# Kernel tuning notes

Hardware: AMD Instinct MI355X
Metric: run time of the kernel (lower is better)

Reference implementation:

```python
import jax, jax.numpy as jnp
import numpy as np

B, N, M, D = 1, 16384, 16384, 3
CHUNK = 2048          # x tile size for the online-min KNN pass
NN_WEIGHT = 1.0       # self.nn_weight
# both_ways=False, free_weight=0, ch_normals_K=0 -> only cham_x branch is active


def setup_inputs() -> dict:
    key = jax.random.key(0)
    k1, k2, k3 = jax.random.split(key, 3)
    # LiDAR-like point clouds, scaled to a ~20 m scene extent
    pc1 = jax.random.normal(k1, (B, N, D), dtype=jnp.float32) * 10.0
    est_flow = jax.random.normal(k2, (B, N, D), dtype=jnp.float32) * 0.1
    pc2 = jax.random.normal(k3, (B, M, D), dtype=jnp.float32) * 10.0
    return {"pc1": pc1, "est_flow": est_flow, "pc2": pc2}


def _knn1_l1_dists(x, y):
    """Per-point min L1 distance from x [N,3] to y [M,3], tiled over x.

    Equivalent to knn_points(x, y, K=1, norm=1).dists[..., 0] without
    materializing the full [N, M] distance matrix.
    """
    n = x.shape[0]
    x_tiles = x.reshape(n // CHUNK, CHUNK, D)

    def tile_min(xc):  # xc: [CHUNK, 3]
        d = jnp.sum(jnp.abs(xc[:, None, :] - y[None, :, :]), axis=-1)  # [CHUNK, M]
        return jnp.min(d, axis=-1)                                     # [CHUNK]

    return jax.lax.map(tile_min, x_tiles).reshape(n)


def reference(pc1, est_flow, pc2):
    x = pc1 + est_flow                                   # deformed cloud [B,N,3]
    cham_x = jax.vmap(_knn1_l1_dists)(x, pc2)            # [B, N]
    cham_y = jnp.float32(0.0)                            # both_ways=False
    freespace_loss = jnp.zeros_like(cham_x)              # free_weight == 0 branch
    chamf_loss = NN_WEIGHT * (cham_x.mean() + cham_y)    # free_weight * 0 omitted
    return (chamf_loss, freespace_loss)
```

## Files before the change

### kernel.cpp

```cpp
#include <hip/hip_runtime.h>


#define TPB 256
#define RB 8
#define PTS_PER_BLOCK (TPB * RB)
#define YSEG 128

__device__ __forceinline__ float rl(float v, int l) {
    return __uint_as_float((unsigned)__builtin_amdgcn_readlane((int)__float_as_uint(v), l));
}

#define DIST2S(MR, AXv, AYv, AZv, Y0X, Y0Y, Y0Z, Y1X, Y1Y, Y1Z)           \
  {                                                                        \
    float t0, t1, t2, t3, t4;                                              \
    asm("v_sub_f32 %1, %9, %6\n\t"                                         \
        "v_sub_f32 %2, %10, %7\n\t"                                        \
        "v_sub_f32 %3, %11, %8\n\t"                                        \
        "v_sub_f32 %4, %12, %6\n\t"                                        \
        "v_sub_f32 %5, %13, %7\n\t"                                        \
        "v_add_f32 %1, |%1|, |%2|\n\t"                                     \
        "v_sub_f32 %2, %14, %8\n\t"                                        \
        "v_add_f32 %4, |%4|, |%5|\n\t"                                     \
        "v_add_f32 %1, %1, |%3|\n\t"                                       \
        "v_add_f32 %4, %4, |%2|\n\t"                                       \
        "v_min3_f32 %0, %0, %1, %4"                                        \
        : "+v"(MR), "=&v"(t0), "=&v"(t1), "=&v"(t2), "=&v"(t3), "=&v"(t4)  \
        : "v"(AXv), "v"(AYv), "v"(AZv),                                    \
          "s"(Y0X), "s"(Y0Y), "s"(Y0Z), "s"(Y1X), "s"(Y1Y), "s"(Y1Z));    \
  }

__global__ __launch_bounds__(TPB) void init_kernel(unsigned* __restrict__ minbits, int N) {
    const int i = blockIdx.x * TPB + threadIdx.x;
    uint4* p = (uint4*)minbits;
    if (i < N / 4) p[i] = make_uint4(0x7F7F7F7Fu, 0x7F7F7F7Fu, 0x7F7F7F7Fu, 0x7F7F7F7Fu);
    for (int k = (N / 4) * 4 + i; k < N; k += 1) { if (i == 0) minbits[k] = 0x7F7F7F7Fu; }
}

__global__ __launch_bounds__(TPB) void chamfer_kernel(
    const float* __restrict__ pc1, const float* __restrict__ flow,
    const float* __restrict__ pc2, unsigned* __restrict__ minbits,
    int N, int M) {
    const int t    = threadIdx.x;
    const int lane = t & 63;

    const int ibase = blockIdx.x * PTS_PER_BLOCK + t;
    float ax[RB], ay[RB], az[RB];
#pragma unroll
    for (int r = 0; r < RB; ++r) {
        const int i = ibase + r * TPB;
        const int ic = (i < N) ? i : (N - 1);
        ax[r] = pc1[3 * ic]     + flow[3 * ic];
        ay[r] = pc1[3 * ic + 1] + flow[3 * ic + 1];
        az[r] = pc1[3 * ic + 2] + flow[3 * ic + 2];
    }

    float m[RB];
#pragma unroll
    for (int r = 0; r < RB; ++r) m[r] = 3.0e38f;

    const int ybase = blockIdx.y * YSEG;
    const int yend  = (ybase + YSEG < M) ? (ybase + YSEG) : M;
    const int nph   = (yend - ybase + 63) >> 6;

    int g = ybase + lane; if (g >= M) g = M - 1;
    float cyx = pc2[3 * g], cyy = pc2[3 * g + 1], cyz = pc2[3 * g + 2];

    for (int p = 0; p < nph; ++p) {
        float nyx, nyy, nyz;
        const bool more = (p + 1 < nph);
        if (more) {
            int h = ybase + (p + 1) * 64 + lane; if (h >= M) h = M - 1;
            nyx = pc2[3 * h]; nyy = pc2[3 * h + 1]; nyz = pc2[3 * h + 2];
        }
#pragma unroll
        for (int j = 0; j < 64; j += 2) {
            const float y0x = rl(cyx, j),     y0y = rl(cyy, j),     y0z = rl(cyz, j);
            const float y1x = rl(cyx, j + 1), y1y = rl(cyy, j + 1), y1z = rl(cyz, j + 1);
#pragma unroll
            for (int r = 0; r < RB; ++r) {
                DIST2S(m[r], ax[r], ay[r], az[r], y0x, y0y, y0z, y1x, y1y, y1z);
            }
        }
        if (more) { cyx = nyx; cyy = nyy; cyz = nyz; }
    }

#pragma unroll
    for (int r = 0; r < RB; ++r) {
        const int i = ibase + r * TPB;
        if (i < N) atomicMin(&minbits[i], __float_as_uint(m[r]));
    }
}

__global__ __launch_bounds__(1024) void reduce_kernel(
    const unsigned* __restrict__ minbits, float* __restrict__ out,
    int N, int out_size) {
    float4* o4 = (float4*)out;
    const int n4 = out_size / 4;
    for (int k = threadIdx.x; k < n4; k += 1024)
        o4[k] = make_float4(0.f, 0.f, 0.f, 0.f);
    for (int k = n4 * 4 + threadIdx.x; k < out_size; k += 1024)
        out[k] = 0.f;

    float s = 0.0f;
    const uint4* p = (const uint4*)minbits;
    for (int k = threadIdx.x; k < N / 4; k += 1024) {
        uint4 v = p[k];
        s += __uint_as_float(v.x) + __uint_as_float(v.y) +
             __uint_as_float(v.z) + __uint_as_float(v.w);
    }
    for (int k = (N / 4) * 4 + threadIdx.x; k < N; k += 1024)
        s += __uint_as_float(minbits[k]);
#pragma unroll
    for (int off = 32; off > 0; off >>= 1) s += __shfl_down(s, off, 64);
    __shared__ float ls[16];
    const int wid = threadIdx.x >> 6, lane = threadIdx.x & 63;
    if (lane == 0) ls[wid] = s;
    __syncthreads();
    if (threadIdx.x == 0) {
        float tot = 0.0f;
        for (int w = 0; w < 16; ++w) tot += ls[w];
        out[0] = tot / (float)N;
    }
}

extern "C" void kernel_launch(void* const* d_in, const int* in_sizes, int n_in,
                              void* d_out, int out_size, void* d_ws, size_t ws_size,
                              hipStream_t stream) {
    const float* pc1  = (const float*)d_in[0];
    const float* flow = (const float*)d_in[1];
    const float* pc2  = (const float*)d_in[2];
    float* out = (float*)d_out;

    const int N = in_sizes[0] / 3;
    const int M = in_sizes[2] / 3;

    unsigned* minbits = (unsigned*)d_ws;

    const int nbN    = (N + PTS_PER_BLOCK - 1) / PTS_PER_BLOCK;
    const int msplit = (M + YSEG - 1) / YSEG;

    init_kernel<<<(N / 4 + TPB - 1) / TPB, TPB, 0, stream>>>(minbits, N);
    chamfer_kernel<<<dim3(nbN, msplit), TPB, 0, stream>>>(pc1, flow, pc2, minbits, N, M);
    reduce_kernel<<<1, 1024, 0, stream>>>(minbits, out, N, out_size);
}
```

Before: 49.21 us.

## Stream y points via double-buffered scalar loads instead of readlane broadcasts

Replaces per-wave vector loads of y points followed by v_readlane broadcasts with double-buffered s_load_dwordx16/x8 scalar loads, which bring 8 y points at a time straight into SGPRs for the distance asm. It also halves the y segment per block (which doubles atomics and re-reads of x) and adds an occupancy hint to launch bounds. Readlane costs and VGPR-to-SGPR traffic go away. In exchange there is hand-managed lgkmcnt waiting, more blocks, and a scalar fallback path for partial segments. The init kernel drops its tail handling, which assumes N is divisible by 4.

Result: faster. 48.18 us (-2.1%).

```diff
diff --git a/kernel.cpp b/kernel.cpp
--- a/kernel.cpp
+++ b/kernel.cpp
@@ -4,11 +4,19 @@
 #define TPB 256
 #define RB 8
 #define PTS_PER_BLOCK (TPB * RB)
-#define YSEG 128
+#define YSEG 64
+#define NITER (YSEG / 16)
 
-__device__ __forceinline__ float rl(float v, int l) {
-    return __uint_as_float((unsigned)__builtin_amdgcn_readlane((int)__float_as_uint(v), l));
-}
+typedef float sf16 __attribute__((ext_vector_type(16)));
+typedef float sf8  __attribute__((ext_vector_type(8)));
+
+#define SLOAD24(B16, B8, PTR, O16, O8)                                     \
+  asm volatile("s_load_dwordx16 %0, %2, " O16 "\n\t"                       \
+               "s_load_dwordx8  %1, %2, " O8                               \
+               : "=s"(B16), "=s"(B8) : "s"(PTR));
+
+#define SWAIT(B16, B8)                                                     \
+  asm volatile("s_waitcnt lgkmcnt(0)" : "+s"(B16), "+s"(B8));
 
 #define DIST2S(MR, AXv, AYv, AZv, Y0X, Y0Y, Y0Z, Y1X, Y1Y, Y1Z)           \
   {                                                                        \
@@ -29,19 +37,37 @@
           "s"(Y0X), "s"(Y0Y), "s"(Y0Z), "s"(Y1X), "s"(Y1Y), "s"(Y1Z));    \
   }
 
-__global__ __launch_bounds__(TPB) void init_kernel(unsigned* __restrict__ minbits, int N) {
+#define COMPUTE8(G16, G8)                                                  \
+  {                                                                        \
+    _Pragma("unroll")                                                      \
+    for (int r = 0; r < RB; ++r)                                           \
+      DIST2S(m[r], ax[r], ay[r], az[r],                                    \
+             G16[0], G16[1], G16[2], G16[3], G16[4], G16[5]);              \
+    _Pragma("unroll")                                                      \
+    for (int r = 0; r < RB; ++r)                                           \
+      DIST2S(m[r], ax[r], ay[r], az[r],                                    \
+             G16[6], G16[7], G16[8], G16[9], G16[10], G16[11]);            \
+    _Pragma("unroll")                                                      \
+    for (int r = 0; r < RB; ++r)                                           \
+      DIST2S(m[r], ax[r], ay[r], az[r],                                    \
+             G16[12], G16[13], G16[14], G16[15], G8[0], G8[1]);            \
+    _Pragma("unroll")                                                      \
+    for (int r = 0; r < RB; ++r)                                           \
+      DIST2S(m[r], ax[r], ay[r], az[r],                                    \
+             G8[2], G8[3], G8[4], G8[5], G8[6], G8[7]);                    \
+  }
+
+__global__ __launch_bounds__(TPB) void init_kernel(unsigned* __restrict__ minbits, int N4) {
     const int i = blockIdx.x * TPB + threadIdx.x;
     uint4* p = (uint4*)minbits;
-    if (i < N / 4) p[i] = make_uint4(0x7F7F7F7Fu, 0x7F7F7F7Fu, 0x7F7F7F7Fu, 0x7F7F7F7Fu);
-    for (int k = (N / 4) * 4 + i; k < N; k += 1) { if (i == 0) minbits[k] = 0x7F7F7F7Fu; }
+    if (i < N4) p[i] = make_uint4(0x7F7F7F7Fu, 0x7F7F7F7Fu, 0x7F7F7F7Fu, 0x7F7F7F7Fu);
 }
 
-__global__ __launch_bounds__(TPB) void chamfer_kernel(
+__global__ __launch_bounds__(TPB, 8) void chamfer_kernel(
     const float* __restrict__ pc1, const float* __restrict__ flow,
     const float* __restrict__ pc2, unsigned* __restrict__ minbits,
     int N, int M) {
-    const int t    = threadIdx.x;
-    const int lane = t & 63;
+    const int t = threadIdx.x;
 
     const int ibase = blockIdx.x * PTS_PER_BLOCK + t;
     float ax[RB], ay[RB], az[RB];
@@ -60,28 +86,29 @@
 
     const int ybase = blockIdx.y * YSEG;
     const int yend  = (ybase + YSEG < M) ? (ybase + YSEG) : M;
-    const int nph   = (yend - ybase + 63) >> 6;
 
-    int g = ybase + lane; if (g >= M) g = M - 1;
-    float cyx = pc2[3 * g], cyy = pc2[3 * g + 1], cyz = pc2[3 * g + 2];
-
-    for (int p = 0; p < nph; ++p) {
-        float nyx, nyy, nyz;
-        const bool more = (p + 1 < nph);
-        if (more) {
-            int h = ybase + (p + 1) * 64 + lane; if (h >= M) h = M - 1;
-            nyx = pc2[3 * h]; nyy = pc2[3 * h + 1]; nyz = pc2[3 * h + 2];
+    if (yend - ybase == YSEG) {
+        const float* yp = pc2 + (size_t)3 * (size_t)ybase;
+        sf16 A16, B16; sf8 A8, B8;
+        SLOAD24(A16, A8, yp, "0", "64");
+#pragma unroll 1
+        for (int it = 0; it < NITER; ++it) {
+            SWAIT(A16, A8);
+            SLOAD24(B16, B8, yp, "96", "160");
+            COMPUTE8(A16, A8);
+            SWAIT(B16, B8);
+            if (it + 1 < NITER)
+                SLOAD24(A16, A8, yp, "192", "256");
+            COMPUTE8(B16, B8);
+            yp += 48;
         }
+    } else {
+        for (int j = ybase; j < yend; ++j) {
+            const float yx = pc2[3 * j], yy = pc2[3 * j + 1], yz = pc2[3 * j + 2];
 #pragma unroll
-        for (int j = 0; j < 64; j += 2) {
-            const float y0x = rl(cyx, j),     y0y = rl(cyy, j),     y0z = rl(cyz, j);
-            const float y1x = rl(cyx, j + 1), y1y = rl(cyy, j + 1), y1z = rl(cyz, j + 1);
-#pragma unroll
-            for (int r = 0; r < RB; ++r) {
-                DIST2S(m[r], ax[r], ay[r], az[r], y0x, y0y, y0z, y1x, y1y, y1z);
-            }
+            for (int r = 0; r < RB; ++r)
+                m[r] = fminf(m[r], fabsf(ax[r] - yx) + fabsf(ay[r] - yy) + fabsf(az[r] - yz));
         }
-        if (more) { cyx = nyx; cyy = nyy; cyz = nyz; }
     }
 
 #pragma unroll
@@ -139,7 +166,7 @@
     const int nbN    = (N + PTS_PER_BLOCK - 1) / PTS_PER_BLOCK;
     const int msplit = (M + YSEG - 1) / YSEG;
 
-    init_kernel<<<(N / 4 + TPB - 1) / TPB, TPB, 0, stream>>>(minbits, N);
+    init_kernel<<<(N / 4 + TPB - 1) / TPB, TPB, 0, stream>>>(minbits, N / 4);
     chamfer_kernel<<<dim3(nbN, msplit), TPB, 0, stream>>>(pc1, flow, pc2, minbits, N, M);
     reduce_kernel<<<1, 1024, 0, stream>>>(minbits, out, N, out_size);
 }
```
